# Kernel tuning notes

Hardware: AMD Instinct MI355X
Metric: run time of the kernel (lower is better)

The kernel has to match this reference:

```python
import jax, jax.numpy as jnp
import numpy as np

H = 1024      # hidden_size
MEL = 128     # mel_bins
B = 32        # batch
TENC = 512    # encoder time steps
TMEL = 400    # decoder (mel) time steps


def setup_inputs() -> dict:
    key = jax.random.key(0)
    ks = jax.random.split(key, 16)
    def w(k, shape, s=0.02):
        return jax.random.normal(k, shape, dtype=jnp.float32) * s
    return dict(
        encoder_hidden=w(ks[0], (4, B, H), 0.1),
        encoder_outputs=w(ks[1], (B, TENC, H), 0.1),
        y=w(ks[2], (B, TMEL, MEL), 1.0),
        mel_spec_lens=jax.random.randint(ks[3], (B,), 1, TMEL),
        # attention linear
        W_attn=w(ks[4], (H, H)), b_attn=jnp.zeros((H,), jnp.float32),
        # GRU layer 0 (input MEL) and layer 1 (input H); gate order r,z,n as in torch
        W_ih0=w(ks[5], (3 * H, MEL)), W_hh0=w(ks[6], (3 * H, H)),
        b_ih0=jnp.zeros((3 * H,), jnp.float32), b_hh0=jnp.zeros((3 * H,), jnp.float32),
        W_ih1=w(ks[7], (3 * H, H)), W_hh1=w(ks[8], (3 * H, H)),
        b_ih1=jnp.zeros((3 * H,), jnp.float32), b_hh1=jnp.zeros((3 * H,), jnp.float32),
        # concat2hidden, mel projection, eos gate
        Wc=w(ks[9], (H, 2 * H)), bc=jnp.zeros((H,), jnp.float32),
        Wp=w(ks[10], (MEL, H)), bp=jnp.zeros((MEL,), jnp.float32),
        Wg=w(ks[11], (1, H)), bg=jnp.zeros((1,), jnp.float32),
    )


def gru_cell(x, h, Wih, Whh, bih, bhh):
    # torch GRUCell math: gates ordered (r, z, n)
    gi = x @ Wih.T + bih          # [B, 3H]
    gh = h @ Whh.T + bhh          # [B, 3H]
    ir, iz, inn = jnp.split(gi, 3, axis=-1)
    hr, hz, hn = jnp.split(gh, 3, axis=-1)
    r = jax.nn.sigmoid(ir + hr)
    z = jax.nn.sigmoid(iz + hz)
    n = jnp.tanh(inn + r * hn)
    return (1.0 - z) * n + z * h


def reference(encoder_hidden, encoder_outputs, y, mel_spec_lens,
              W_attn, b_attn,
              W_ih0, W_hh0, b_ih0, b_hh0,
              W_ih1, W_hh1, b_ih1, b_hh1,
              Wc, bc, Wp, bp, Wg, bg):
    Bsz, Tmel, mel = y.shape
    # attention energy depends only on encoder_outputs -> hoist out of the loop (same math)
    energy = encoder_outputs @ W_attn.T + b_attn          # [B, Te, H]
    h0 = encoder_hidden[0]                                 # decoder_hidden = encoder_hidden[:num_layers]
    h1 = encoder_hidden[1]
    dec_in0 = jnp.zeros((Bsz, mel), y.dtype)               # SOS frame

    def step(carry, _):
        dec_in, h0, h1 = carry
        h0 = gru_cell(dec_in, h0, W_ih0, W_hh0, b_ih0, b_hh0)
        h1 = gru_cell(h0, h1, W_ih1, W_hh1, b_ih1, b_hh1)   # rnn_output = top-layer state [B, H]
        scores = jnp.einsum('bh,bth->bt', h1, energy)       # additive-style dot scores [B, Te]
        probs = jax.nn.softmax(scores, axis=1)
        context = jnp.einsum('bt,bth->bh', probs, encoder_outputs)  # [B, H]
        co = jnp.tanh(jnp.concatenate([h1, context], axis=-1) @ Wc.T + bc)  # [B, H]
        mel_out = co @ Wp.T + bp                            # [B, MEL]
        gate = (co @ Wg.T + bg)[:, 0]                       # [B]
        return (mel_out, h0, h1), (mel_out, gate)

    _, (mels, gates) = jax.lax.scan(step, (dec_in0, h0, h1), None, length=Tmel)
    mels = jnp.transpose(mels, (1, 0, 2))                   # [B, T, MEL]
    gates = gates.T                                          # [B, T]

    t = jnp.arange(Tmel)
    mask = t[None, :] > mel_spec_lens[:, None]               # strictly-greater, as in source
    masked_mel = jnp.where(mask[:, :, None], 0.0, mels)
    masked_gate = jnp.where(mask, 1000.0, gates)
    return masked_mel, masked_gate, mask
```

## Files before the change

### kernel.cpp

```cpp
#include <hip/hip_runtime.h>
#include <stdint.h>
#include <stddef.h>


#define TM 400

typedef unsigned short ushort_t;
typedef unsigned long long u64_t;
typedef short    short8  __attribute__((ext_vector_type(8)));
typedef float    float4v __attribute__((ext_vector_type(4)));
typedef unsigned uint2v  __attribute__((ext_vector_type(2)));

#define DEVI static __device__ __forceinline__

#define SB_WF   0
#define SB_IH1  3145728
#define SB_HH0  6291456
#define SB_HH1  9437184
#define SB_AT   12582912
#define SB_WC   13631488
#define SB_WP   15728640
#define SW_TOT  15859712

__device__ __align__(16) ushort_t g_sw[SW_TOT];
__device__ __align__(16) float    g_wf[3145728];
__device__ __align__(16) ushort_t g_encb[16777216];
__device__ __align__(16) unsigned char g_en8[16777216];
__device__ __align__(16) unsigned char g_ec8[16777216];
__device__ __align__(16) ushort_t g_h0b[32768], g_h1b[32768];
__device__ __align__(16) float    g_h0f[32768], g_h1f[32768];
__device__ __align__(16) float    g_b0f[3072];
__device__ __align__(16) float    g_gh0[98304], g_gh1[98304];
__device__ __align__(16) float    g_ctxn[32768], g_sden[32];
__device__ __align__(16) float    g_cof[32768];
__device__ __align__(16) ushort_t g_cob[32768];
__device__ __align__(64) unsigned g_done[16];

DEVI ushort_t f2b(float f) {
  union { float f; uint32_t u; } c; c.f = f;
  uint32_t u = c.u + 0x7fffu + ((c.u >> 16) & 1u);
  return (ushort_t)(u >> 16);
}
DEVI float sigm(float x) { return 1.f / (1.f + __expf(-x)); }

DEVI unsigned char f2e4m3(float f) {
  union { float f; uint32_t u; } c; c.f = f;
  const unsigned s = (c.u >> 24) & 0x80u;
  const float a = fabsf(f);
  if (a >= 448.f) return (unsigned char)(s | 0x7Eu);
  if (a < 0.015625f) {
    int m = (int)(a * 512.f + 0.5f);
    if (m >= 8) return (unsigned char)(s | 0x08u);
    return (unsigned char)(s | (unsigned)m);
  }
  int e32 = (int)((c.u >> 23) & 0xffu);
  uint32_t m3 = (c.u >> 20) & 7u;
  const uint32_t rem = c.u & 0xfffffu;
  if (rem > 0x80000u || (rem == 0x80000u && (m3 & 1u))) {
    if (++m3 == 8u) { m3 = 0u; ++e32; }
  }
  const int e8 = e32 - 120;
  if (e8 >= 16) return (unsigned char)(s | 0x7Eu);
  return (unsigned char)(s | ((unsigned)e8 << 3) | m3);
}

DEVI float4v mfma16(short8 a, short8 b, float4v c) {
  return __builtin_amdgcn_mfma_f32_16x16x32_bf16(a, b, c, 0, 0, 0);
}

DEVI u64_t ld_sc8(const void* p) {
  return __hip_atomic_load((const u64_t*)p, __ATOMIC_RELAXED,
                           __HIP_MEMORY_SCOPE_SYSTEM);
}
DEVI float ld_scf(const float* p) {
  return __hip_atomic_load(p, __ATOMIC_RELAXED, __HIP_MEMORY_SCOPE_SYSTEM);
}

DEVI float4v gemm_plain(const ushort_t* Ab, const ushort_t* Bw,
                        int ntile, int mu, int lane) {
  float4v acc = {0.f, 0.f, 0.f, 0.f};
  const ushort_t* a = Ab + (size_t)(mu * 16 + (lane & 15)) * 1024 + ((lane >> 4) << 3);
  const ushort_t* b = Bw + ((size_t)ntile * 32 * 64 + lane) * 8;
  for (int kb = 0; kb < 32; ++kb) {
    short8 av = *(const short8*)(a + kb * 32);
    acc = mfma16(av, *(const short8*)(b + (size_t)kb * 512), acc);
  }
  return acc;
}

DEVI float4v gemm_scE2(const ushort_t* h1b, const float* ctxn, const float* sden,
                       const ushort_t* Bw, int ntile, int mu, int lane) {
  float4v acc = {0.f, 0.f, 0.f, 0.f};
  const int m = mu * 16 + (lane & 15), ko = (lane >> 4) << 3;
  const ushort_t* a0 = h1b + (size_t)m * 1024 + ko;
  const float* a1 = ctxn + (size_t)m * 1024 + ko;
  const float den = ld_scf(&sden[m]);
  const float inv = (den > 1e-35f) ? (1.f / den) : 0.f;
  const ushort_t* b = Bw + ((size_t)ntile * 64 * 64 + lane) * 8;
  for (int kb = 0; kb < 32; ++kb)
    acc = mfma16(*(const short8*)(a0 + kb * 32),
                 *(const short8*)(b + (size_t)kb * 512), acc);
  for (int c = 0; c < 4; ++c) {
    u64_t t[32];
#pragma unroll
    for (int j = 0; j < 8; ++j)
#pragma unroll
      for (int q = 0; q < 4; ++q)
        t[j * 4 + q] = ld_sc8(a1 + (c * 8 + j) * 32 + q * 2);
#pragma unroll
    for (int j = 0; j < 8; ++j) {
      short8 av;
#pragma unroll
      for (int q = 0; q < 4; ++q) {
        union { u64_t u; float f[2]; } w; w.u = t[j * 4 + q];
        av[q * 2]     = (short)f2b(w.f[0] * inv);
        av[q * 2 + 1] = (short)f2b(w.f[1] * inv);
      }
      acc = mfma16(av, *(const short8*)(b + (size_t)(32 + c * 8 + j) * 512), acc);
    }
  }
  return acc;
}

DEVI void put_tile(float* sh, int q, int lane, float4v a) {
  const int base = q * 256 + (lane & 15);
#pragma unroll
  for (int i = 0; i < 4; ++i) sh[base + ((lane >> 4) * 4 + i) * 16] = a[i];
}

__global__ void k_wf(const float* __restrict__ Wih0, const float* __restrict__ Wp) {
  __shared__ __align__(16) float As[32][128];
  __shared__ __align__(16) float Bs[128][64];
  const int tid = threadIdx.x;
  const int nt = blockIdx.x >> 4, kt = blockIdx.x & 15;
  const int n0 = nt * 32, k0 = kt * 64;
  {
    const int r = tid >> 3, c0 = (tid & 7) * 16;
    for (int i = 0; i < 16; i += 4)
      *(float4v*)&As[r][c0 + i] = *(const float4v*)&Wih0[(size_t)(n0 + r) * 128 + c0 + i];
  }
  {
    const int r = tid >> 1, c0 = (tid & 1) * 32;
    for (int i = 0; i < 32; i += 4)
      *(float4v*)&Bs[r][c0 + i] = *(const float4v*)&Wp[(size_t)r * 1024 + k0 + c0 + i];
  }
  __syncthreads();
  const int rn = tid >> 3, kq = (tid & 7) * 8;
  float acc[8] = {0.f, 0.f, 0.f, 0.f, 0.f, 0.f, 0.f, 0.f};
  for (int m = 0; m < 128; ++m) {
    const float a = As[rn][m];
#pragma unroll
    for (int j = 0; j < 8; ++j) acc[j] += a * Bs[m][kq + j];
  }
  float* dst = g_wf + (size_t)(n0 + rn) * 1024 + k0 + kq;
#pragma unroll
  for (int j = 0; j < 8; ++j) dst[j] = acc[j];
}

__global__ void k_encb(const float* __restrict__ enc) {
  const size_t i = ((size_t)blockIdx.x * 256 + threadIdx.x) * 8;
  if (i >= 16777216) return;
  float4v a = *(const float4v*)(enc + i);
  float4v b = *(const float4v*)(enc + i + 4);
  short8 r;
#pragma unroll
  for (int j = 0; j < 4; ++j) { r[j] = (short)f2b(a[j]); r[4 + j] = (short)f2b(b[j]); }
  *(short8*)(g_encb + i) = r;
}

__global__ void k_q8(const float* __restrict__ enc) {
  const size_t i = ((size_t)blockIdx.x * 256 + threadIdx.x) * 8;
  if (i >= 16777216) return;
  float4v a = *(const float4v*)(enc + i);
  float4v b = *(const float4v*)(enc + i + 4);
  unsigned lo = 0, hi = 0;
#pragma unroll
  for (int j = 0; j < 4; ++j) {
    lo |= (unsigned)f2e4m3(a[j]) << (8 * j);
    hi |= (unsigned)f2e4m3(b[j]) << (8 * j);
  }
  uint2v o; o[0] = lo; o[1] = hi;
  *(uint2v*)(g_ec8 + i) = o;
}

__global__ void k_swz(const float* __restrict__ W1, const float* __restrict__ W2,
                      const float* __restrict__ W3, const float* __restrict__ WA,
                      const float* __restrict__ WC, const float* __restrict__ Wp) {
  long fid = (long)blockIdx.x * 256 + threadIdx.x;
  if (fid >= 1982464) return;
  const float* src; int N, K; long base, local;
  if      (fid < 393216)  { src = g_wf; N = 3072; K = 1024; base = SB_WF;  local = fid; }
  else if (fid < 786432)  { src = W1;   N = 3072; K = 1024; base = SB_IH1; local = fid - 393216; }
  else if (fid < 1179648) { src = W2;   N = 3072; K = 1024; base = SB_HH0; local = fid - 786432; }
  else if (fid < 1572864) { src = W3;   N = 3072; K = 1024; base = SB_HH1; local = fid - 1179648; }
  else if (fid < 1703936) { src = WA;   N = 1024; K = 1024; base = SB_AT;  local = fid - 1572864; }
  else if (fid < 1966080) { src = WC;   N = 1024; K = 2048; base = SB_WC;  local = fid - 1703936; }
  else                    { src = Wp;   N = 128;  K = 1024; base = SB_WP;  local = fid - 1966080; }
  const int L = (int)(local & 63);
  long rest = local >> 6;
  const int KB = K >> 5;
  const int kb = (int)(rest % KB);
  const int nt = (int)(rest / KB);
  const int n  = nt * 16 + (L & 15);
  const int k0 = kb * 32 + ((L >> 4) << 3);
  short8 r;
#pragma unroll
  for (int i = 0; i < 8; ++i)
    r[i] = (short)f2b(src[(size_t)n * K + (k0 + i)]);
  *(short8*)(g_sw + base + local * 8) = r;
}

__global__ void k_energy(const float* __restrict__ b_attn) {
  __shared__ __align__(16) float sh[2048];
  const int tid = threadIdx.x, lane = tid & 63, wv = tid >> 6;
  const int rt = blockIdx.x;
  const ushort_t* Ab = g_encb + (size_t)rt * 32 * 1024;
  float* shw = sh + wv * 512;
  for (int i = 0; i < 16; ++i) {
    const int nt = wv * 16 + i;
    put_tile(shw, 0, lane, gemm_plain(Ab, g_sw + SB_AT, nt, 0, lane));
    put_tile(shw, 1, lane, gemm_plain(Ab, g_sw + SB_AT, nt, 1, lane));
    __syncthreads();
    const int row = lane >> 1, cf = (lane & 1) * 8;
    const int q = row >> 4, r = row & 15;
    unsigned lo = 0, hi = 0;
#pragma unroll
    for (int j = 0; j < 4; ++j) {
      lo |= (unsigned)f2e4m3(shw[q * 256 + r * 16 + cf + j] + b_attn[nt * 16 + cf + j]) << (8 * j);
      hi |= (unsigned)f2e4m3(shw[q * 256 + r * 16 + cf + 4 + j] + b_attn[nt * 16 + cf + 4 + j]) << (8 * j);
    }
    uint2v o; o[0] = lo; o[1] = hi;
    *(uint2v*)(g_en8 + (size_t)(rt * 32 + row) * 1024 + nt * 16 + cf) = o;
    __syncthreads();
  }
}

__global__ void k_init(const float* __restrict__ ehid, const int* __restrict__ lens,
                       const float* __restrict__ Wih0, const float* __restrict__ bp,
                       const float* __restrict__ bih0,
                       float* __restrict__ out, int out_size) {
  int i = blockIdx.x * 256 + threadIdx.x;
  if (i == 0) g_done[0] = 0u;
  if (i < 32768) { float v = ehid[i]; g_h0f[i] = v; g_h0b[i] = f2b(v); }
  else if (i < 65536) {
    int j = i - 32768; float v = ehid[32768 + j];
    g_h1f[j] = v; g_h1b[j] = f2b(v);
  } else if (i < 78336) {
    int mi = i - 65536; int b = mi / 400, tt = mi % 400;
    int idx = 1651200 + mi;
    if (idx < out_size) out[idx] = (tt > lens[b]) ? 1.0f : 0.0f;
  } else if (i < 81408) {
    int n = i - 78336;
    float s = bih0[n];
    const float* wr = Wih0 + (size_t)n * 128;
    for (int m = 0; m < 128; ++m) s += bp[m] * wr[m];
    g_b0f[n] = s;
  }
}

__global__ void k_pre(const float* __restrict__ b_hh0, const float* __restrict__ b_hh1) {
  const int wg = blockIdx.x, tid = threadIdx.x;
  const int lane = tid & 63, wv = tid >> 6;
  __shared__ __align__(16) float sh[1536];
  const int qa = (wv < 2) ? wv * 2 : wv + 2;
  const int qb = (wv < 2) ? wv * 2 + 1 : -1;
  const ushort_t* Ab = (wg < 64) ? g_h0b : g_h1b;
  const ushort_t* Bw = g_sw + ((wg < 64) ? SB_HH0 : SB_HH1);
  const float* bhh = (wg < 64) ? b_hh0 : b_hh1;
  float* ghb = (wg < 64) ? g_gh0 : g_gh1;
  const int w16 = wg & 63;
  { int g = qa >> 1, mu = qa & 1;
    put_tile(sh, qa, lane, gemm_plain(Ab, Bw, g * 64 + w16, mu, lane)); }
  if (qb >= 0) { int g = qb >> 1, mu = qb & 1;
    put_tile(sh, qb, lane, gemm_plain(Ab, Bw, g * 64 + w16, mu, lane)); }
  __syncthreads();
  const int jl = tid & 15, mr = tid >> 4, jg = w16 * 16 + jl;
#pragma unroll
  for (int mu = 0; mu < 2; ++mu) {
    const int b = mu * 16 + mr;
#pragma unroll
    for (int g = 0; g < 3; ++g)
      ghb[b * 3072 + g * 1024 + jg] = sh[(g * 2 + mu) * 256 + tid] + bhh[g * 1024 + jg];
  }
}

__global__ void k_s1(int t, const float* __restrict__ b_ih0, const float* __restrict__ bp,
                     const float* __restrict__ Wg, const float* __restrict__ bg,
                     const int* __restrict__ lens,
                     float* __restrict__ out, int out_size) {
  const int wg = blockIdx.x, tid = threadIdx.x;
  const int lane = tid & 63, wv = tid >> 6;
  __shared__ __align__(16) float sh[1536];
  if (wg < 64) {
    if (t >= TM) return;
    const int qa = (wv < 2) ? wv * 2 : wv + 2;
    const int qb = (wv < 2) ? wv * 2 + 1 : -1;
    const ushort_t* SW = g_sw + SB_WF;
    float4v acc;
    { int g = qa >> 1, mu = qa & 1;
      acc = (t > 0) ? gemm_plain(g_cob, SW, g * 64 + wg, mu, lane)
                    : float4v{0.f, 0.f, 0.f, 0.f};
      put_tile(sh, qa, lane, acc); }
    if (qb >= 0) { int g = qb >> 1, mu = qb & 1;
      acc = (t > 0) ? gemm_plain(g_cob, SW, g * 64 + wg, mu, lane)
                    : float4v{0.f, 0.f, 0.f, 0.f};
      put_tile(sh, qb, lane, acc); }
    __syncthreads();
    const int jl = tid & 15, mr = tid >> 4, jg = wg * 16 + jl;
    const float* bs = (t > 0) ? g_b0f : b_ih0;
    const float bir = bs[jg], biz = bs[1024 + jg], bin = bs[2048 + jg];
#pragma unroll
    for (int mu = 0; mu < 2; ++mu) {
      const int b = mu * 16 + mr;
      float gr = sh[mu * 256 + tid]       + bir + g_gh0[b * 3072 + jg];
      float gz = sh[(2 + mu) * 256 + tid] + biz + g_gh0[b * 3072 + 1024 + jg];
      float gn = sh[(4 + mu) * 256 + tid] + bin;
      float r = sigm(gr), z = sigm(gz);
      float nn = tanhf(gn + r * g_gh0[b * 3072 + 2048 + jg]);
      float h = (1.f - z) * nn + z * g_h0f[b * 1024 + jg];
      g_h0f[b * 1024 + jg] = h; g_h0b[b * 1024 + jg] = f2b(h);
    }
  } else if (wg < 72) {
    if (t == 0) return;
    const int nt = wg - 64;
    if (wv < 2)
      put_tile(sh, wv, lane, gemm_plain(g_cob, g_sw + SB_WP, nt, wv, lane));
    __syncthreads();
    const int jl = tid & 15, mr = tid >> 4;
    const int m = nt * 16 + jl;
    const float bpv = bp[m];
#pragma unroll
    for (int mu = 0; mu < 2; ++mu) {
      const int b = mu * 16 + mr;
      const bool mk = (t - 1) > lens[b];
      const float v = mk ? 0.f : (sh[mu * 256 + tid] + bpv);
      const int oidx = b * 51200 + (t - 1) * 128 + m;
      if (oidx < out_size) out[oidx] = v;
    }
  } else if (wg == 72) {
    if (t == 0) return;
    const int b = tid >> 3, seg = tid & 7;
    const float* cop = g_cof + b * 1024 + seg * 128;
    const float* wgp = Wg + seg * 128;
    float s = 0.f;
#pragma unroll 8
    for (int k = 0; k < 128; k += 4) {
      float4v cv = *(const float4v*)(cop + k);
      float4v wv4 = *(const float4v*)(wgp + k);
      s += cv[0] * wv4[0] + cv[1] * wv4[1] + cv[2] * wv4[2] + cv[3] * wv4[3];
    }
    for (int o = 1; o < 8; o <<= 1) s += __shfl_xor(s, o, 64);
    if (seg == 0) {
      const bool mk = (t - 1) > lens[b];
      const float g = mk ? 1000.f : (s + bg[0]);
      const int oidx = 1638400 + b * 400 + (t - 1);
      if (oidx < out_size) out[oidx] = g;
    }
  } else {
    const int z0 = (wg - 73) * 256 + tid;
#pragma unroll
    for (int r4 = 0; r4 < 16; ++r4) g_ctxn[z0 + r4 * 2048] = 0.f;
    if (wg == 73 && tid < 32) g_sden[tid] = 0.f;
    if (wg == 73 && tid == 0)
      __hip_atomic_store(&g_done[0], 0u, __ATOMIC_RELAXED,
                         __HIP_MEMORY_SCOPE_AGENT);
  }
}

__global__ void k_s2(const float* __restrict__ b_ih1, const float* __restrict__ b_hh0) {
  const int wg = blockIdx.x, tid = threadIdx.x;
  const int lane = tid & 63, wv = tid >> 6;
  __shared__ __align__(16) float sh[1536];
  const int qa = (wv < 2) ? wv * 2 : wv + 2;
  const int qb = (wv < 2) ? wv * 2 + 1 : -1;
  const bool lo = (wg < 64);
  const int w16 = wg & 63;
  const ushort_t* SW = g_sw + (lo ? SB_IH1 : SB_HH0);
  { int g = qa >> 1, mu = qa & 1;
    put_tile(sh, qa, lane, gemm_plain(g_h0b, SW, g * 64 + w16, mu, lane)); }
  if (qb >= 0) { int g = qb >> 1, mu = qb & 1;
    put_tile(sh, qb, lane, gemm_plain(g_h0b, SW, g * 64 + w16, mu, lane)); }
  __syncthreads();
  const int jl = tid & 15, mr = tid >> 4, jg = w16 * 16 + jl;
  if (lo) {
    const float bir = b_ih1[jg], biz = b_ih1[1024 + jg], bin = b_ih1[2048 + jg];
#pragma unroll
    for (int mu = 0; mu < 2; ++mu) {
      const int b = mu * 16 + mr;
      float gr = sh[mu * 256 + tid]       + bir + g_gh1[b * 3072 + jg];
      float gz = sh[(2 + mu) * 256 + tid] + biz + g_gh1[b * 3072 + 1024 + jg];
      float gn = sh[(4 + mu) * 256 + tid] + bin;
      float r = sigm(gr), z = sigm(gz);
      float nn = tanhf(gn + r * g_gh1[b * 3072 + 2048 + jg]);
      float h = (1.f - z) * nn + z * g_h1f[b * 1024 + jg];
      g_h1f[b * 1024 + jg] = h; g_h1b[b * 1024 + jg] = f2b(h);
    }
  } else {
#pragma unroll
    for (int mu = 0; mu < 2; ++mu) {
      const int b = mu * 16 + mr;
#pragma unroll
      for (int g = 0; g < 3; ++g)
        g_gh0[b * 3072 + g * 1024 + jg] = sh[(g * 2 + mu) * 256 + tid] + b_hh0[g * 1024 + jg];
    }
  }
}

__global__ void k_s34(const float* __restrict__ bc, const float* __restrict__ b_hh1) {
  __shared__ __align__(16) float sh[4160];
  __shared__ __align__(16) float tabf[256];
  const int wg = blockIdx.x, tid = threadIdx.x;
  const int lane = tid & 63, wv = tid >> 6;
  if (wg < 256) {
    {
      const unsigned v = (unsigned)tid;
      const unsigned e = (v >> 3) & 0xFu, m = v & 7u;
      union { unsigned u; float f; } c;
      if (e == 0u) c.f = (float)m * 0.001953125f;
      else c.u = ((e + 120u) << 23) | (m << 20);
      c.u |= (v & 0x80u) << 24;
      tabf[v] = c.f;
    }
    const int b = wg >> 3, slot = wg & 7;
    const float* hp = g_h1f + b * 1024;
    float u0[8], u1[8];
    {
      float4v a0 = *(const float4v*)(hp + lane * 8);
      float4v a1 = *(const float4v*)(hp + lane * 8 + 4);
      float4v b0 = *(const float4v*)(hp + 512 + lane * 8);
      float4v b1 = *(const float4v*)(hp + 512 + lane * 8 + 4);
#pragma unroll
      for (int j = 0; j < 4; ++j) {
        u0[j] = a0[j]; u0[4 + j] = a1[j];
        u1[j] = b0[j]; u1[4 + j] = b1[j];
      }
    }
    __syncthreads();
    float cx0[8] = {0.f, 0.f, 0.f, 0.f, 0.f, 0.f, 0.f, 0.f};
    float cx1[8] = {0.f, 0.f, 0.f, 0.f, 0.f, 0.f, 0.f, 0.f};
    float sw = 0.f;
    const size_t base = ((size_t)(b * 512 + slot * 64 + wv * 16)) * 1024 + lane * 8;
    for (int it = 0; it < 16; ++it) {
      const size_t off = base + (size_t)it * 1024;
      uint2v gE0 = *(const uint2v*)(g_en8 + off);
      uint2v gE1 = *(const uint2v*)(g_en8 + off + 512);
      uint2v eE0 = *(const uint2v*)(g_ec8 + off);
      uint2v eE1 = *(const uint2v*)(g_ec8 + off + 512);
      float ef0[8], ef1[8];
      float s = 0.f;
#pragma unroll
      for (int w = 0; w < 2; ++w)
#pragma unroll
        for (int j = 0; j < 4; ++j) {
          const int k = w * 4 + j;
          s += u0[k] * tabf[(gE0[w] >> (8 * j)) & 0xffu];
          s += u1[k] * tabf[(gE1[w] >> (8 * j)) & 0xffu];
          ef0[k] = tabf[(eE0[w] >> (8 * j)) & 0xffu];
          ef1[k] = tabf[(eE1[w] >> (8 * j)) & 0xffu];
        }
      for (int o = 1; o < 64; o <<= 1) s += __shfl_xor(s, o, 64);
      const float sc = fminf(fmaxf(s, -70.f), 70.f);
      const float p = __expf(sc);
      sw += p;
#pragma unroll
      for (int j = 0; j < 8; ++j) { cx0[j] += p * ef0[j]; cx1[j] += p * ef1[j]; }
    }
#pragma unroll
    for (int j = 0; j < 8; ++j) {
      sh[wv * 1024 + lane * 8 + j]       = cx0[j];
      sh[wv * 1024 + 512 + lane * 8 + j] = cx1[j];
    }
    if (lane == 0) sh[4096 + wv] = sw;
    __syncthreads();
    float4v t4 = {0.f, 0.f, 0.f, 0.f};
#pragma unroll
    for (int v = 0; v < 4; ++v) t4 += *(const float4v*)&sh[v * 1024 + tid * 4];
    float* dst = g_ctxn + b * 1024 + tid * 4;
#pragma unroll
    for (int c = 0; c < 4; ++c) unsafeAtomicAdd(dst + c, t4[c]);
    if (tid == 0)
      unsafeAtomicAdd(&g_sden[b], sh[4096] + sh[4097] + sh[4098] + sh[4099]);
    __syncthreads();
    if (tid == 0)
      __hip_atomic_fetch_add(&g_done[0], 1u, __ATOMIC_RELAXED,
                             __HIP_MEMORY_SCOPE_AGENT);
  } else if (wg < 320) {
    const int w16 = wg - 256;
    if (tid == 0) {
      unsigned spins = 0;
      while (__hip_atomic_load(&g_done[0], __ATOMIC_RELAXED,
                               __HIP_MEMORY_SCOPE_AGENT) < 256u) {
        __builtin_amdgcn_s_sleep(2);
        if (++spins > (1u << 22)) break;
      }
    }
    __syncthreads();
    if (wv < 2)
      put_tile(sh, wv, lane, gemm_scE2(g_h1b, g_ctxn, g_sden, g_sw + SB_WC, w16, wv, lane));
    __syncthreads();
    const int jl = tid & 15, mr = tid >> 4;
    const float bcv = bc[w16 * 16 + jl];
#pragma unroll
    for (int mu = 0; mu < 2; ++mu) {
      const int b = mu * 16 + mr;
      const float v = tanhf(sh[mu * 256 + tid] + bcv);
      g_cof[b * 1024 + w16 * 16 + jl] = v;
      g_cob[b * 1024 + w16 * 16 + jl] = f2b(v);
    }
  } else {
    const int w16 = wg - 320;
    const int qa = (wv < 2) ? wv * 2 : wv + 2;
    const int qb = (wv < 2) ? wv * 2 + 1 : -1;
    { int g = qa >> 1, mu = qa & 1;
      put_tile(sh, qa, lane, gemm_plain(g_h1b, g_sw + SB_HH1, g * 64 + w16, mu, lane)); }
    if (qb >= 0) { int g = qb >> 1, mu = qb & 1;
      put_tile(sh, qb, lane, gemm_plain(g_h1b, g_sw + SB_HH1, g * 64 + w16, mu, lane)); }
    __syncthreads();
    const int jl = tid & 15, mr = tid >> 4, jg = w16 * 16 + jl;
#pragma unroll
    for (int mu = 0; mu < 2; ++mu) {
      const int b = mu * 16 + mr;
#pragma unroll
      for (int g = 0; g < 3; ++g)
        g_gh1[b * 3072 + g * 1024 + jg] = sh[(g * 2 + mu) * 256 + tid] + b_hh1[g * 1024 + jg];
    }
  }
}

extern "C" void kernel_launch(void* const* d_in, const int* in_sizes, int n_in,
                              void* d_out, int out_size, void* d_ws, size_t ws_size,
                              hipStream_t stream) {
  const float* ehid  = (const float*)d_in[0];
  const float* enc   = (const float*)d_in[1];
  const int*   lens  = (const int*)d_in[3];
  const float* W_attn= (const float*)d_in[4];
  const float* b_attn= (const float*)d_in[5];
  const float* W_ih0 = (const float*)d_in[6];
  const float* W_hh0 = (const float*)d_in[7];
  const float* b_ih0 = (const float*)d_in[8];
  const float* b_hh0 = (const float*)d_in[9];
  const float* W_ih1 = (const float*)d_in[10];
  const float* W_hh1 = (const float*)d_in[11];
  const float* b_ih1 = (const float*)d_in[12];
  const float* b_hh1 = (const float*)d_in[13];
  const float* Wc    = (const float*)d_in[14];
  const float* bc    = (const float*)d_in[15];
  const float* Wp    = (const float*)d_in[16];
  const float* bp    = (const float*)d_in[17];
  const float* Wg    = (const float*)d_in[18];
  const float* bg    = (const float*)d_in[19];
  float* out = (float*)d_out;

  k_wf    <<<1536, 256, 0, stream>>>(W_ih0, Wp);
  k_encb  <<<8192, 256, 0, stream>>>(enc);
  k_q8    <<<8192, 256, 0, stream>>>(enc);
  k_swz   <<<7744, 256, 0, stream>>>(W_ih1, W_hh0, W_hh1, W_attn, Wc, Wp);
  k_energy<<<512,  256, 0, stream>>>(b_attn);
  k_init  <<<318,  256, 0, stream>>>(ehid, lens, W_ih0, bp, b_ih0, out, out_size);
  k_pre   <<<128,  256, 0, stream>>>(b_hh0, b_hh1);
  for (int t = 0; t < TM; ++t) {
    k_s1 <<<81,  256, 0, stream>>>(t, b_ih0, bp, Wg, bg, lens, out, out_size);
    k_s2 <<<128, 256, 0, stream>>>(b_ih1, b_hh0);
    k_s34<<<384, 256, 0, stream>>>(bc, b_hh1);
  }
  k_s1<<<81, 256, 0, stream>>>(TM, b_ih0, bp, Wg, bg, lens, out, out_size);
}
```

Baseline: 24.69 ms.

## Fuse per-step kernels into one launch with counter-based intra-kernel dependencies

```diff
diff --git a/kernel.cpp b/kernel.cpp
--- a/kernel.cpp
+++ b/kernel.cpp
@@ -9,7 +9,6 @@
 typedef unsigned long long u64_t;
 typedef short    short8  __attribute__((ext_vector_type(8)));
 typedef float    float4v __attribute__((ext_vector_type(4)));
-typedef unsigned uint2v  __attribute__((ext_vector_type(2)));
 
 #define DEVI static __device__ __forceinline__
 
@@ -25,8 +24,7 @@
 __device__ __align__(16) ushort_t g_sw[SW_TOT];
 __device__ __align__(16) float    g_wf[3145728];
 __device__ __align__(16) ushort_t g_encb[16777216];
-__device__ __align__(16) unsigned char g_en8[16777216];
-__device__ __align__(16) unsigned char g_ec8[16777216];
+__device__ __align__(16) ushort_t g_energy[16777216];
 __device__ __align__(16) ushort_t g_h0b[32768], g_h1b[32768];
 __device__ __align__(16) float    g_h0f[32768], g_h1f[32768];
 __device__ __align__(16) float    g_b0f[3072];
@@ -34,35 +32,17 @@
 __device__ __align__(16) float    g_ctxn[32768], g_sden[32];
 __device__ __align__(16) float    g_cof[32768];
 __device__ __align__(16) ushort_t g_cob[32768];
-__device__ __align__(64) unsigned g_done[16];
+__device__ __align__(64) unsigned g_cnt[64];
 
 DEVI ushort_t f2b(float f) {
   union { float f; uint32_t u; } c; c.f = f;
   uint32_t u = c.u + 0x7fffu + ((c.u >> 16) & 1u);
   return (ushort_t)(u >> 16);
 }
+DEVI float b2f(ushort_t b) {
+  union { uint32_t u; float f; } c; c.u = ((uint32_t)b) << 16; return c.f;
+}
 DEVI float sigm(float x) { return 1.f / (1.f + __expf(-x)); }
-
-DEVI unsigned char f2e4m3(float f) {
-  union { float f; uint32_t u; } c; c.f = f;
-  const unsigned s = (c.u >> 24) & 0x80u;
-  const float a = fabsf(f);
-  if (a >= 448.f) return (unsigned char)(s | 0x7Eu);
-  if (a < 0.015625f) {
-    int m = (int)(a * 512.f + 0.5f);
-    if (m >= 8) return (unsigned char)(s | 0x08u);
-    return (unsigned char)(s | (unsigned)m);
-  }
-  int e32 = (int)((c.u >> 23) & 0xffu);
-  uint32_t m3 = (c.u >> 20) & 7u;
-  const uint32_t rem = c.u & 0xfffffu;
-  if (rem > 0x80000u || (rem == 0x80000u && (m3 & 1u))) {
-    if (++m3 == 8u) { m3 = 0u; ++e32; }
-  }
-  const int e8 = e32 - 120;
-  if (e8 >= 16) return (unsigned char)(s | 0x7Eu);
-  return (unsigned char)(s | ((unsigned)e8 << 3) | m3);
-}
 
 DEVI float4v mfma16(short8 a, short8 b, float4v c) {
   return __builtin_amdgcn_mfma_f32_16x16x32_bf16(a, b, c, 0, 0, 0);
@@ -74,6 +54,25 @@
 }
 DEVI float ld_scf(const float* p) {
   return __hip_atomic_load(p, __ATOMIC_RELAXED, __HIP_MEMORY_SCOPE_SYSTEM);
+}
+DEVI void st_scf(float* p, float v) {
+  __hip_atomic_store(p, v, __ATOMIC_RELAXED, __HIP_MEMORY_SCOPE_SYSTEM);
+}
+DEVI void st_scu(unsigned* p, unsigned v) {
+  __hip_atomic_store(p, v, __ATOMIC_RELAXED, __HIP_MEMORY_SCOPE_SYSTEM);
+}
+DEVI void bump(unsigned* ctr) {
+  __hip_atomic_fetch_add(ctr, 1u, __ATOMIC_RELAXED, __HIP_MEMORY_SCOPE_AGENT);
+}
+DEVI unsigned ldc(const unsigned* ctr) {
+  return __hip_atomic_load(ctr, __ATOMIC_RELAXED, __HIP_MEMORY_SCOPE_AGENT);
+}
+DEVI void spin1(const unsigned* c, unsigned tgt) {
+  unsigned sp = 0;
+  while (ldc(c) < tgt) {
+    __builtin_amdgcn_s_sleep(2);
+    if (++sp > (1u << 22)) break;
+  }
 }
 
 DEVI float4v gemm_plain(const ushort_t* Ab, const ushort_t* Bw,
@@ -88,8 +87,29 @@
   return acc;
 }
 
-DEVI float4v gemm_scE2(const ushort_t* h1b, const float* ctxn, const float* sden,
-                       const ushort_t* Bw, int ntile, int mu, int lane) {
+DEVI float4v gemm_sc(const ushort_t* Ab, const ushort_t* Bw,
+                     int ntile, int mu, int lane) {
+  float4v acc = {0.f, 0.f, 0.f, 0.f};
+  const ushort_t* a = Ab + (size_t)(mu * 16 + (lane & 15)) * 1024 + ((lane >> 4) << 3);
+  const ushort_t* b = Bw + ((size_t)ntile * 32 * 64 + lane) * 8;
+  for (int c = 0; c < 2; ++c) {
+    u64_t lo[16], hi[16];
+#pragma unroll
+    for (int j = 0; j < 16; ++j) {
+      lo[j] = ld_sc8(a + (c * 16 + j) * 32);
+      hi[j] = ld_sc8(a + (c * 16 + j) * 32 + 4);
+    }
+#pragma unroll
+    for (int j = 0; j < 16; ++j) {
+      union { u64_t u[2]; short8 s; } cv; cv.u[0] = lo[j]; cv.u[1] = hi[j];
+      acc = mfma16(cv.s, *(const short8*)(b + (size_t)(c * 16 + j) * 512), acc);
+    }
+  }
+  return acc;
+}
+
+DEVI float4v gemm_co(const ushort_t* h1b, const float* ctxn, const float* sden,
+                     const ushort_t* Bw, int ntile, int mu, int lane) {
   float4v acc = {0.f, 0.f, 0.f, 0.f};
   const int m = mu * 16 + (lane & 15), ko = (lane >> 4) << 3;
   const ushort_t* a0 = h1b + (size_t)m * 1024 + ko;
@@ -97,9 +117,19 @@
   const float den = ld_scf(&sden[m]);
   const float inv = (den > 1e-35f) ? (1.f / den) : 0.f;
   const ushort_t* b = Bw + ((size_t)ntile * 64 * 64 + lane) * 8;
-  for (int kb = 0; kb < 32; ++kb)
-    acc = mfma16(*(const short8*)(a0 + kb * 32),
-                 *(const short8*)(b + (size_t)kb * 512), acc);
+  for (int c = 0; c < 2; ++c) {
+    u64_t lo[16], hi[16];
+#pragma unroll
+    for (int j = 0; j < 16; ++j) {
+      lo[j] = ld_sc8(a0 + (c * 16 + j) * 32);
+      hi[j] = ld_sc8(a0 + (c * 16 + j) * 32 + 4);
+    }
+#pragma unroll
+    for (int j = 0; j < 16; ++j) {
+      union { u64_t u[2]; short8 s; } cv; cv.u[0] = lo[j]; cv.u[1] = hi[j];
+      acc = mfma16(cv.s, *(const short8*)(b + (size_t)(c * 16 + j) * 512), acc);
+    }
+  }
   for (int c = 0; c < 4; ++c) {
     u64_t t[32];
 #pragma unroll
@@ -166,21 +196,6 @@
 #pragma unroll
   for (int j = 0; j < 4; ++j) { r[j] = (short)f2b(a[j]); r[4 + j] = (short)f2b(b[j]); }
   *(short8*)(g_encb + i) = r;
-}
-
-__global__ void k_q8(const float* __restrict__ enc) {
-  const size_t i = ((size_t)blockIdx.x * 256 + threadIdx.x) * 8;
-  if (i >= 16777216) return;
-  float4v a = *(const float4v*)(enc + i);
-  float4v b = *(const float4v*)(enc + i + 4);
-  unsigned lo = 0, hi = 0;
-#pragma unroll
-  for (int j = 0; j < 4; ++j) {
-    lo |= (unsigned)f2e4m3(a[j]) << (8 * j);
-    hi |= (unsigned)f2e4m3(b[j]) << (8 * j);
-  }
-  uint2v o; o[0] = lo; o[1] = hi;
-  *(uint2v*)(g_ec8 + i) = o;
 }
 
 __global__ void k_swz(const float* __restrict__ W1, const float* __restrict__ W2,
@@ -223,14 +238,13 @@
     __syncthreads();
     const int row = lane >> 1, cf = (lane & 1) * 8;
     const int q = row >> 4, r = row & 15;
-    unsigned lo = 0, hi = 0;
-#pragma unroll
-    for (int j = 0; j < 4; ++j) {
-      lo |= (unsigned)f2e4m3(shw[q * 256 + r * 16 + cf + j] + b_attn[nt * 16 + cf + j]) << (8 * j);
-      hi |= (unsigned)f2e4m3(shw[q * 256 + r * 16 + cf + 4 + j] + b_attn[nt * 16 + cf + 4 + j]) << (8 * j);
-    }
-    uint2v o; o[0] = lo; o[1] = hi;
-    *(uint2v*)(g_en8 + (size_t)(rt * 32 + row) * 1024 + nt * 16 + cf) = o;
+    short8 o;
+#pragma unroll
+    for (int j = 0; j < 8; ++j) {
+      const int n = nt * 16 + cf + j;
+      o[j] = (short)f2b(shw[q * 256 + r * 16 + cf + j] + b_attn[n]);
+    }
+    *(short8*)(g_energy + (size_t)(rt * 32 + row) * 1024 + nt * 16 + cf) = o;
     __syncthreads();
   }
 }
@@ -240,7 +254,7 @@
                        const float* __restrict__ bih0,
                        float* __restrict__ out, int out_size) {
   int i = blockIdx.x * 256 + threadIdx.x;
-  if (i == 0) g_done[0] = 0u;
+  if (i < 64) g_cnt[i] = 0u;
   if (i < 32768) { float v = ehid[i]; g_h0f[i] = v; g_h0b[i] = f2b(v); }
   else if (i < 65536) {
     int j = i - 32768; float v = ehid[32768 + j];
@@ -284,15 +298,17 @@
   }
 }
 
-__global__ void k_s1(int t, const float* __restrict__ b_ih0, const float* __restrict__ bp,
-                     const float* __restrict__ Wg, const float* __restrict__ bg,
-                     const int* __restrict__ lens,
-                     float* __restrict__ out, int out_size) {
+__global__ void __launch_bounds__(256) k_step(
+    int t,
+    const float* __restrict__ b_ih0, const float* __restrict__ b_ih1,
+    const float* __restrict__ b_hh0, const float* __restrict__ b_hh1,
+    const float* __restrict__ bc, const float* __restrict__ bp,
+    const float* __restrict__ Wg, const float* __restrict__ bg,
+    const int* __restrict__ lens, float* __restrict__ out, int out_size) {
+  __shared__ __align__(16) float sh[4160];
   const int wg = blockIdx.x, tid = threadIdx.x;
   const int lane = tid & 63, wv = tid >> 6;
-  __shared__ __align__(16) float sh[1536];
   if (wg < 64) {
-    if (t >= TM) return;
     const int qa = (wv < 2) ? wv * 2 : wv + 2;
     const int qb = (wv < 2) ? wv * 2 + 1 : -1;
     const ushort_t* SW = g_sw + SB_WF;
@@ -318,8 +334,15 @@
       float r = sigm(gr), z = sigm(gz);
       float nn = tanhf(gn + r * g_gh0[b * 3072 + 2048 + jg]);
       float h = (1.f - z) * nn + z * g_h0f[b * 1024 + jg];
-      g_h0f[b * 1024 + jg] = h; g_h0b[b * 1024 + jg] = f2b(h);
-    }
+      g_h0f[b * 1024 + jg] = h;
+      ushort_t hb = f2b(h);
+      ushort_t hb1 = (ushort_t)__shfl_down((int)hb, 1, 64);
+      if (!(jl & 1))
+        st_scu((unsigned*)&g_h0b[b * 1024 + jg],
+               (unsigned)hb | ((unsigned)hb1 << 16));
+    }
+    __syncthreads();
+    if (tid == 0) bump(&g_cnt[0]);
   } else if (wg < 72) {
     if (t == 0) return;
     const int nt = wg - 64;
@@ -356,33 +379,26 @@
       const int oidx = 1638400 + b * 400 + (t - 1);
       if (oidx < out_size) out[oidx] = g;
     }
-  } else {
+  } else if (wg < 81) {
     const int z0 = (wg - 73) * 256 + tid;
 #pragma unroll
-    for (int r4 = 0; r4 < 16; ++r4) g_ctxn[z0 + r4 * 2048] = 0.f;
-    if (wg == 73 && tid < 32) g_sden[tid] = 0.f;
-    if (wg == 73 && tid == 0)
-      __hip_atomic_store(&g_done[0], 0u, __ATOMIC_RELAXED,
-                         __HIP_MEMORY_SCOPE_AGENT);
-  }
-}
-
-__global__ void k_s2(const float* __restrict__ b_ih1, const float* __restrict__ b_hh0) {
-  const int wg = blockIdx.x, tid = threadIdx.x;
-  const int lane = tid & 63, wv = tid >> 6;
-  __shared__ __align__(16) float sh[1536];
-  const int qa = (wv < 2) ? wv * 2 : wv + 2;
-  const int qb = (wv < 2) ? wv * 2 + 1 : -1;
-  const bool lo = (wg < 64);
-  const int w16 = wg & 63;
-  const ushort_t* SW = g_sw + (lo ? SB_IH1 : SB_HH0);
-  { int g = qa >> 1, mu = qa & 1;
-    put_tile(sh, qa, lane, gemm_plain(g_h0b, SW, g * 64 + w16, mu, lane)); }
-  if (qb >= 0) { int g = qb >> 1, mu = qb & 1;
-    put_tile(sh, qb, lane, gemm_plain(g_h0b, SW, g * 64 + w16, mu, lane)); }
-  __syncthreads();
-  const int jl = tid & 15, mr = tid >> 4, jg = w16 * 16 + jl;
-  if (lo) {
+    for (int r4 = 0; r4 < 16; ++r4) st_scf(&g_ctxn[z0 + r4 * 2048], 0.f);
+    if (wg == 73 && tid < 32) st_scf(&g_sden[tid], 0.f);
+    __syncthreads();
+    if (tid == 0) bump(&g_cnt[32]);
+  } else if (wg < 145) {
+    const int w16 = wg - 81;
+    if (tid == 0) spin1(&g_cnt[0], (unsigned)(t + 1) * 64u);
+    __syncthreads();
+    const int qa = (wv < 2) ? wv * 2 : wv + 2;
+    const int qb = (wv < 2) ? wv * 2 + 1 : -1;
+    const ushort_t* SW = g_sw + SB_IH1;
+    { int g = qa >> 1, mu = qa & 1;
+      put_tile(sh, qa, lane, gemm_sc(g_h0b, SW, g * 64 + w16, mu, lane)); }
+    if (qb >= 0) { int g = qb >> 1, mu = qb & 1;
+      put_tile(sh, qb, lane, gemm_sc(g_h0b, SW, g * 64 + w16, mu, lane)); }
+    __syncthreads();
+    const int jl = tid & 15, mr = tid >> 4, jg = w16 * 16 + jl;
     const float bir = b_ih1[jg], biz = b_ih1[1024 + jg], bin = b_ih1[2048 + jg];
 #pragma unroll
     for (int mu = 0; mu < 2; ++mu) {
@@ -393,9 +409,28 @@
       float r = sigm(gr), z = sigm(gz);
       float nn = tanhf(gn + r * g_gh1[b * 3072 + 2048 + jg]);
       float h = (1.f - z) * nn + z * g_h1f[b * 1024 + jg];
-      g_h1f[b * 1024 + jg] = h; g_h1b[b * 1024 + jg] = f2b(h);
-    }
-  } else {
+      st_scf(&g_h1f[b * 1024 + jg], h);
+      ushort_t hb = f2b(h);
+      ushort_t hb1 = (ushort_t)__shfl_down((int)hb, 1, 64);
+      if (!(jl & 1))
+        st_scu((unsigned*)&g_h1b[b * 1024 + jg],
+               (unsigned)hb | ((unsigned)hb1 << 16));
+    }
+    __syncthreads();
+    if (tid == 0) bump(&g_cnt[16]);
+  } else if (wg < 209) {
+    const int w16 = wg - 145;
+    if (tid == 0) spin1(&g_cnt[0], (unsigned)(t + 1) * 64u);
+    __syncthreads();
+    const int qa = (wv < 2) ? wv * 2 : wv + 2;
+    const int qb = (wv < 2) ? wv * 2 + 1 : -1;
+    const ushort_t* SW = g_sw + SB_HH0;
+    { int g = qa >> 1, mu = qa & 1;
+      put_tile(sh, qa, lane, gemm_sc(g_h0b, SW, g * 64 + w16, mu, lane)); }
+    if (qb >= 0) { int g = qb >> 1, mu = qb & 1;
+      put_tile(sh, qb, lane, gemm_sc(g_h0b, SW, g * 64 + w16, mu, lane)); }
+    __syncthreads();
+    const int jl = tid & 15, mr = tid >> 4, jg = w16 * 16 + jl;
 #pragma unroll
     for (int mu = 0; mu < 2; ++mu) {
       const int b = mu * 16 + mr;
@@ -403,61 +438,46 @@
       for (int g = 0; g < 3; ++g)
         g_gh0[b * 3072 + g * 1024 + jg] = sh[(g * 2 + mu) * 256 + tid] + b_hh0[g * 1024 + jg];
     }
-  }
-}
-
-__global__ void k_s34(const float* __restrict__ bc, const float* __restrict__ b_hh1) {
-  __shared__ __align__(16) float sh[4160];
-  __shared__ __align__(16) float tabf[256];
-  const int wg = blockIdx.x, tid = threadIdx.x;
-  const int lane = tid & 63, wv = tid >> 6;
-  if (wg < 256) {
-    {
-      const unsigned v = (unsigned)tid;
-      const unsigned e = (v >> 3) & 0xFu, m = v & 7u;
-      union { unsigned u; float f; } c;
-      if (e == 0u) c.f = (float)m * 0.001953125f;
-      else c.u = ((e + 120u) << 23) | (m << 20);
-      c.u |= (v & 0x80u) << 24;
-      tabf[v] = c.f;
-    }
-    const int b = wg >> 3, slot = wg & 7;
+  } else if (wg < 465) {
+    const int a = wg - 209, b = a >> 3, slot = a & 7;
+    if (tid == 0) {
+      spin1(&g_cnt[16], (unsigned)(t + 1) * 64u);
+      spin1(&g_cnt[32], (unsigned)(t + 1) * 8u);
+    }
+    __syncthreads();
     const float* hp = g_h1f + b * 1024;
     float u0[8], u1[8];
     {
-      float4v a0 = *(const float4v*)(hp + lane * 8);
-      float4v a1 = *(const float4v*)(hp + lane * 8 + 4);
-      float4v b0 = *(const float4v*)(hp + 512 + lane * 8);
-      float4v b1 = *(const float4v*)(hp + 512 + lane * 8 + 4);
+      union { u64_t u; float f[2]; } tt;
 #pragma unroll
       for (int j = 0; j < 4; ++j) {
-        u0[j] = a0[j]; u0[4 + j] = a1[j];
-        u1[j] = b0[j]; u1[4 + j] = b1[j];
+        tt.u = ld_sc8(hp + lane * 8 + j * 2);
+        u0[j * 2] = tt.f[0]; u0[j * 2 + 1] = tt.f[1];
       }
-    }
-    __syncthreads();
+#pragma unroll
+      for (int j = 0; j < 4; ++j) {
+        tt.u = ld_sc8(hp + 512 + lane * 8 + j * 2);
+        u1[j * 2] = tt.f[0]; u1[j * 2 + 1] = tt.f[1];
+      }
+    }
     float cx0[8] = {0.f, 0.f, 0.f, 0.f, 0.f, 0.f, 0.f, 0.f};
     float cx1[8] = {0.f, 0.f, 0.f, 0.f, 0.f, 0.f, 0.f, 0.f};
     float sw = 0.f;
     const size_t base = ((size_t)(b * 512 + slot * 64 + wv * 16)) * 1024 + lane * 8;
     for (int it = 0; it < 16; ++it) {
       const size_t off = base + (size_t)it * 1024;
-      uint2v gE0 = *(const uint2v*)(g_en8 + off);
-      uint2v gE1 = *(const uint2v*)(g_en8 + off + 512);
-      uint2v eE0 = *(const uint2v*)(g_ec8 + off);
-      uint2v eE1 = *(const uint2v*)(g_ec8 + off + 512);
+      short8 g0 = *(const short8*)(g_energy + off);
+      short8 g1 = *(const short8*)(g_energy + off + 512);
+      short8 e0 = *(const short8*)(g_encb + off);
+      short8 e1 = *(const short8*)(g_encb + off + 512);
       float ef0[8], ef1[8];
       float s = 0.f;
 #pragma unroll
-      for (int w = 0; w < 2; ++w)
-#pragma unroll
-        for (int j = 0; j < 4; ++j) {
-          const int k = w * 4 + j;
-          s += u0[k] * tabf[(gE0[w] >> (8 * j)) & 0xffu];
-          s += u1[k] * tabf[(gE1[w] >> (8 * j)) & 0xffu];
-          ef0[k] = tabf[(eE0[w] >> (8 * j)) & 0xffu];
-          ef1[k] = tabf[(eE1[w] >> (8 * j)) & 0xffu];
-        }
+      for (int j = 0; j < 8; ++j) {
+        ef0[j] = b2f((ushort_t)e0[j]);
+        ef1[j] = b2f((ushort_t)e1[j]);
+        s += u0[j] * b2f((ushort_t)g0[j]) + u1[j] * b2f((ushort_t)g1[j]);
+      }
       for (int o = 1; o < 64; o <<= 1) s += __shfl_xor(s, o, 64);
       const float sc = fminf(fmaxf(s, -70.f), 70.f);
       const float p = __expf(sc);
@@ -481,22 +501,33 @@
     if (tid == 0)
       unsafeAtomicAdd(&g_sden[b], sh[4096] + sh[4097] + sh[4098] + sh[4099]);
     __syncthreads();
-    if (tid == 0)
-      __hip_atomic_fetch_add(&g_done[0], 1u, __ATOMIC_RELAXED,
-                             __HIP_MEMORY_SCOPE_AGENT);
-  } else if (wg < 320) {
-    const int w16 = wg - 256;
-    if (tid == 0) {
-      unsigned spins = 0;
-      while (__hip_atomic_load(&g_done[0], __ATOMIC_RELAXED,
-                               __HIP_MEMORY_SCOPE_AGENT) < 256u) {
-        __builtin_amdgcn_s_sleep(2);
-        if (++spins > (1u << 22)) break;
-      }
-    }
+    if (tid == 0) bump(&g_cnt[48]);
+  } else if (wg < 529) {
+    const int w16 = wg - 465;
+    if (tid == 0) spin1(&g_cnt[16], (unsigned)(t + 1) * 64u);
+    __syncthreads();
+    const int qa = (wv < 2) ? wv * 2 : wv + 2;
+    const int qb = (wv < 2) ? wv * 2 + 1 : -1;
+    const ushort_t* SW = g_sw + SB_HH1;
+    { int g = qa >> 1, mu = qa & 1;
+      put_tile(sh, qa, lane, gemm_sc(g_h1b, SW, g * 64 + w16, mu, lane)); }
+    if (qb >= 0) { int g = qb >> 1, mu = qb & 1;
+      put_tile(sh, qb, lane, gemm_sc(g_h1b, SW, g * 64 + w16, mu, lane)); }
+    __syncthreads();
+    const int jl = tid & 15, mr = tid >> 4, jg = w16 * 16 + jl;
+#pragma unroll
+    for (int mu = 0; mu < 2; ++mu) {
+      const int b = mu * 16 + mr;
+#pragma unroll
+      for (int g = 0; g < 3; ++g)
+        g_gh1[b * 3072 + g * 1024 + jg] = sh[(g * 2 + mu) * 256 + tid] + b_hh1[g * 1024 + jg];
+    }
+  } else {
+    const int w16 = wg - 529;
+    if (tid == 0) spin1(&g_cnt[48], (unsigned)(t + 1) * 256u);
     __syncthreads();
     if (wv < 2)
-      put_tile(sh, wv, lane, gemm_scE2(g_h1b, g_ctxn, g_sden, g_sw + SB_WC, w16, wv, lane));
+      put_tile(sh, wv, lane, gemm_co(g_h1b, g_ctxn, g_sden, g_sw + SB_WC, w16, wv, lane));
     __syncthreads();
     const int jl = tid & 15, mr = tid >> 4;
     const float bcv = bc[w16 * 16 + jl];
@@ -507,22 +538,47 @@
       g_cof[b * 1024 + w16 * 16 + jl] = v;
       g_cob[b * 1024 + w16 * 16 + jl] = f2b(v);
     }
-  } else {
-    const int w16 = wg - 320;
-    const int qa = (wv < 2) ? wv * 2 : wv + 2;
-    const int qb = (wv < 2) ? wv * 2 + 1 : -1;
-    { int g = qa >> 1, mu = qa & 1;
-      put_tile(sh, qa, lane, gemm_plain(g_h1b, g_sw + SB_HH1, g * 64 + w16, mu, lane)); }
-    if (qb >= 0) { int g = qb >> 1, mu = qb & 1;
-      put_tile(sh, qb, lane, gemm_plain(g_h1b, g_sw + SB_HH1, g * 64 + w16, mu, lane)); }
-    __syncthreads();
-    const int jl = tid & 15, mr = tid >> 4, jg = w16 * 16 + jl;
+  }
+}
+
+__global__ void k_fin(const float* __restrict__ bp, const float* __restrict__ Wg,
+                      const float* __restrict__ bg, const int* __restrict__ lens,
+                      float* __restrict__ out, int out_size) {
+  __shared__ __align__(16) float sh[512];
+  const int wg = blockIdx.x, tid = threadIdx.x;
+  const int lane = tid & 63, wv = tid >> 6;
+  if (wg < 8) {
+    if (wv < 2)
+      put_tile(sh, wv, lane, gemm_plain(g_cob, g_sw + SB_WP, wg, wv, lane));
+    __syncthreads();
+    const int jl = tid & 15, mr = tid >> 4;
+    const int m = wg * 16 + jl;
+    const float bpv = bp[m];
 #pragma unroll
     for (int mu = 0; mu < 2; ++mu) {
       const int b = mu * 16 + mr;
-#pragma unroll
-      for (int g = 0; g < 3; ++g)
-        g_gh1[b * 3072 + g * 1024 + jg] = sh[(g * 2 + mu) * 256 + tid] + b_hh1[g * 1024 + jg];
+      const bool mk = (TM - 1) > lens[b];
+      const float v = mk ? 0.f : (sh[mu * 256 + tid] + bpv);
+      const int oidx = b * 51200 + (TM - 1) * 128 + m;
+      if (oidx < out_size) out[oidx] = v;
+    }
+  } else {
+    const int b = tid >> 3, seg = tid & 7;
+    const float* cop = g_cof + b * 1024 + seg * 128;
+    const float* wgp = Wg + seg * 128;
+    float s = 0.f;
+#pragma unroll 8
+    for (int k = 0; k < 128; k += 4) {
+      float4v cv = *(const float4v*)(cop + k);
+      float4v wv4 = *(const float4v*)(wgp + k);
+      s += cv[0] * wv4[0] + cv[1] * wv4[1] + cv[2] * wv4[2] + cv[3] * wv4[3];
+    }
+    for (int o = 1; o < 8; o <<= 1) s += __shfl_xor(s, o, 64);
+    if (seg == 0) {
+      const bool mk = (TM - 1) > lens[b];
+      const float g = mk ? 1000.f : (s + bg[0]);
+      const int oidx = 1638400 + b * 400 + (TM - 1);
+      if (oidx < out_size) out[oidx] = g;
     }
   }
 }
@@ -553,15 +609,12 @@
 
   k_wf    <<<1536, 256, 0, stream>>>(W_ih0, Wp);
   k_encb  <<<8192, 256, 0, stream>>>(enc);
-  k_q8    <<<8192, 256, 0, stream>>>(enc);
   k_swz   <<<7744, 256, 0, stream>>>(W_ih1, W_hh0, W_hh1, W_attn, Wc, Wp);
   k_energy<<<512,  256, 0, stream>>>(b_attn);
   k_init  <<<318,  256, 0, stream>>>(ehid, lens, W_ih0, bp, b_ih0, out, out_size);
   k_pre   <<<128,  256, 0, stream>>>(b_hh0, b_hh1);
-  for (int t = 0; t < TM; ++t) {
-    k_s1 <<<81,  256, 0, stream>>>(t, b_ih0, bp, Wg, bg, lens, out, out_size);
-    k_s2 <<<128, 256, 0, stream>>>(b_ih1, b_hh0);
-    k_s34<<<384, 256, 0, stream>>>(bc, b_hh1);
-  }
-  k_s1<<<81, 256, 0, stream>>>(TM, b_ih0, bp, Wg, bg, lens, out, out_size);
-}
+  for (int t = 0; t < TM; ++t)
+    k_step<<<593, 256, 0, stream>>>(t, b_ih0, b_ih1, b_hh0, b_hh1, bc, bp,
+                                    Wg, bg, lens, out, out_size);
+  k_fin<<<9, 256, 0, stream>>>(bp, Wg, bg, lens, out, out_size);
+}
```

New measurement: 41.64 ms. 68.7% more time.
